# Kernel tuning notes

Measured on AMD Instinct MI355X. Metric: run time of the kernel, lower is better.

## Reference

```python
import jax, jax.numpy as jnp
import numpy as np
import math

N_ITERS = 10
N_SPIXELS = 256
NEG_INF = -1e10


def _grid_layout(h, w, n_spixels):
    # init_grid: near-square superpixel grid
    nw = int(math.sqrt(n_spixels * w / h))
    nh = int(math.sqrt(n_spixels * h / w))
    cy = np.minimum((np.arange(h) * nh) // h, nh - 1)
    cx = np.minimum((np.arange(w) * nw) // w, nw - 1)
    iy = np.broadcast_to(cy[:, None], (h, w))
    ix = np.broadcast_to(cx[None, :], (h, w))
    init_idx = iy * nw + ix  # [h,w] hard grid assignment
    # 9 candidate superpixels per pixel (3x3 neighborhood of its grid cell)
    offs = np.array([(dy, dx) for dy in (-1, 0, 1) for dx in (-1, 0, 1)])
    ny = iy[None] + offs[:, 0, None, None]  # [9,h,w]
    nx = ix[None] + offs[:, 1, None, None]
    valid = (ny >= 0) & (ny < nh) & (nx >= 0) & (nx < nw)
    nidx = np.clip(ny, 0, nh - 1) * nw + np.clip(nx, 0, nw - 1)
    return init_idx.astype(np.int32), nidx.astype(np.int32), valid, nw, nh


def setup_inputs() -> dict:
    key = jax.random.key(0)
    x = jax.random.normal(key, (2, 20, 512, 512), dtype=jnp.float32)
    return {"x": x}


def reference(x):
    b, c, h, w = x.shape
    init_idx_np, nidx_np, valid_np, nw, nh = _grid_layout(h, w, N_SPIXELS)
    K = nw * nh
    n = h * w
    init_idx = jnp.asarray(init_idx_np.reshape(n))          # [N]
    nidx = jnp.asarray(nidx_np.reshape(9, n))                # [9,N]
    valid = jnp.asarray(valid_np.reshape(9, n))              # [9,N]
    flat_nidx = nidx.reshape(-1)                             # [9N]

    pf_all = x.reshape(b, c, n)

    def init_spf(pf):  # pf [c,N] -> [c,K]: hard-assignment mean (InitSpixelFeats)
        s = jax.ops.segment_sum(pf.T, init_idx, num_segments=K)      # [K,c]
        cnt = jax.ops.segment_sum(jnp.ones((n,), pf.dtype), init_idx, num_segments=K)
        return (s / jnp.maximum(cnt, 1.0)[:, None]).T

    def calc_neg_dist(pf, spf):  # CalcAssoc: [9,N] neg sq dist to 9 neighbors
        nf = spf[:, nidx]                                    # [c,9,N]
        d = jnp.sum((pf[:, None, :] - nf) ** 2, axis=0)      # [9,N]
        return jnp.where(valid, -d, NEG_INF)

    def map_p2sp(pf, Q):  # CalcSpixelFeats: Q-weighted scatter mean, Q [9,N]
        wf = (pf[:, None, :] * Q[None]).reshape(c, -1)       # [c,9N]
        num = jax.ops.segment_sum(wf.T, flat_nidx, num_segments=K)   # [K,c]
        den = jax.ops.segment_sum(Q.reshape(-1), flat_nidx, num_segments=K)
        return (num / jnp.maximum(den, 1e-8)[:, None]).T

    def per_sample(pf):
        spf0 = init_spf(jax.lax.stop_gradient(pf))  # spf init from detached pf
        Q0 = jnp.zeros((9, n), pf.dtype)
        def body(carry, _):
            spf, _ = carry
            Q = jax.nn.softmax(calc_neg_dist(pf, spf), axis=0)
            return (map_p2sp(pf, Q), Q), None
        (spf, Q), _ = jax.lax.scan(body, (spf0, Q0), None, length=N_ITERS)
        return Q, spf

    Q, spf = jax.vmap(per_sample)(pf_all)
    return Q.reshape(b, 9, h, w), spf, x
```

## Files before the change

kernel.cpp:

```cpp
#include <hip/hip_runtime.h>

#define BATCH 2
#define C 20
#define W 512
#define NPIX (512*512)
#define NW 16
#define NH 16
#define K 256
#define NITERS 10
#define SPLIT 4
#define PITCH 260
#define NEG_INF_F (-1.0e10f)
#define REC 189
#define RECP 192

__global__ __launch_bounds__(256)
void ssn_init_kernel(const float* __restrict__ x,
                     float* __restrict__ outX,
                     float* __restrict__ buf0) {
    __shared__ float pf_tile[C][PITCH];
    __shared__ float chpart[80];
    const int t    = threadIdx.x;
    const int bi   = blockIdx.x;
    const int cell = bi & (K - 1);
    const int b    = bi >> 8;
    const int ky = cell >> 4, kx = cell & 15;
    const int py = t >> 5, px = t & 31;
    const int xcol = kx * 32 + px;

    const float* xb = x    + (size_t)b * C * NPIX;
    float*       ox = outX + (size_t)b * C * NPIX;
    float sum4[C];
#pragma unroll
    for (int ch = 0; ch < C; ++ch) sum4[ch] = 0.f;
#pragma unroll
    for (int p = 0; p < 4; ++p) {
        int y = ky * 32 + p * 8 + py;
        const float* src = xb + (size_t)y * W + xcol;
        float*       dst = ox + (size_t)y * W + xcol;
#pragma unroll
        for (int ch = 0; ch < C; ++ch) {
            float v = src[(size_t)ch * NPIX];
            sum4[ch] += v;
            dst[(size_t)ch * NPIX] = v;
        }
    }
#pragma unroll
    for (int ch = 0; ch < C; ++ch) pf_tile[ch][t] = sum4[ch];
    __syncthreads();
    if (t < 80) {
        int ch = t >> 2, q = t & 3;
        const float4* p = (const float4*)&pf_tile[ch][0];
        float s4 = 0.f;
#pragma unroll
        for (int i = 0; i < 16; ++i) {
            float4 v = p[q * 16 + i];
            s4 += v.x + v.y + v.z + v.w;
        }
        chpart[t] = s4;
    }
    __syncthreads();
    if (t < REC) {
        float v = 0.f;
        if (t >= 84 && t < 104) {
            int ch = t - 84;
            v = chpart[ch * 4] + chpart[ch * 4 + 1]
              + chpart[ch * 4 + 2] + chpart[ch * 4 + 3];
        } else if (t == 104) {
            v = 1024.0f;
        }
        float* base = buf0 + (size_t)bi * (SPLIT * RECP);
        base[t] = v;
        base[RECP + t] = 0.f;
        base[2 * RECP + t] = 0.f;
        base[3 * RECP + t] = 0.f;
    }
}

__global__ __launch_bounds__(256)
void ssn_iterate_kernel(const float* __restrict__ x,
                        const float* __restrict__ rp,
                        float* __restrict__ wp,
                        float* __restrict__ outQ,
                        int last) {
    __shared__ float spf_lds[9][C];
    __shared__ float den_lds[9];
    __shared__ float sumsq_lds[9];
    __shared__ float pf_tile[C][PITCH];
    __shared__ float w_tile[9][PITCH];

    const int t  = threadIdx.x;
    const int bi = blockIdx.x;
    const int s    = bi & 3;
    const int cell = (bi >> 2) & (K - 1);
    const int b    = bi >> 10;
    const int bcell = (b << 8) + cell;
    const int ky = cell >> 4, kx = cell & 15;
    const int py = t >> 5, px = t & 31;
    const int y  = ky * 32 + s * 8 + py;
    const int xcol = kx * 32 + px;

    float pf[C];
    const float* xb = x + (size_t)b * C * NPIX + (size_t)y * W + xcol;
#pragma unroll
    for (int ch = 0; ch < C; ++ch) pf[ch] = xb[(size_t)ch * NPIX];

    float numreg = 0.f;
    if (t < 180) {
        int jj = t / 20, ch = t % 20;
        int ny = ky + jj / 3 - 1, nx = kx + jj % 3 - 1;
        if (ny >= 0 && ny < NH && nx >= 0 && nx < NW) {
#pragma unroll
            for (int j2 = 0; j2 < 9; ++j2) {
                int cy = ny - (j2 / 3 - 1), cx = nx - (j2 % 3 - 1);
                if (cy >= 0 && cy < NH && cx >= 0 && cx < NW) {
                    const float* p = rp +
                        (size_t)((b << 8) + cy * NW + cx) * (SPLIT * RECP)
                        + j2 * 21 + ch;
#pragma unroll
                    for (int ss = 0; ss < SPLIT; ++ss)
                        numreg += p[ss * RECP];
                }
            }
        }
    }
    if (t >= 192 && t < 201) {
        int jj = t - 192;
        int ny = ky + jj / 3 - 1, nx = kx + jj % 3 - 1;
        float den = 0.f;
        if (ny >= 0 && ny < NH && nx >= 0 && nx < NW) {
#pragma unroll
            for (int j2 = 0; j2 < 9; ++j2) {
                int cy = ny - (j2 / 3 - 1), cx = nx - (j2 % 3 - 1);
                if (cy >= 0 && cy < NH && cx >= 0 && cx < NW) {
                    const float* p = rp +
                        (size_t)((b << 8) + cy * NW + cx) * (SPLIT * RECP)
                        + j2 * 21 + 20;
#pragma unroll
                    for (int ss = 0; ss < SPLIT; ++ss)
                        den += p[ss * RECP];
                }
            }
        }
        den_lds[jj] = den;
    }
    __syncthreads();
    if (t < 180) {
        int jj = t / 20, ch = t % 20;
        spf_lds[jj][ch] = numreg / fmaxf(den_lds[jj], 1e-8f);
    }
    __syncthreads();
    if (t < 9) {
        float ss2 = 0.f;
#pragma unroll
        for (int ch = 0; ch < C; ++ch) ss2 += spf_lds[t][ch] * spf_lds[t][ch];
        sumsq_lds[t] = ss2;
    }
    __syncthreads();

    float sc[9];
#pragma unroll
    for (int j = 0; j < 9; ++j) {
        int ny = ky + j / 3 - 1, nx = kx + j % 3 - 1;
        bool valid = (ny >= 0 && ny < NH && nx >= 0 && nx < NW);
        float dot = 0.f;
#pragma unroll
        for (int ch = 0; ch < C; ++ch) dot = fmaf(pf[ch], spf_lds[j][ch], dot);
        sc[j] = valid ? fmaf(2.f, dot, -sumsq_lds[j]) : NEG_INF_F;
    }
    float m = sc[0];
#pragma unroll
    for (int j = 1; j < 9; ++j) m = fmaxf(m, sc[j]);
    float wv[9], wsum = 0.f;
#pragma unroll
    for (int j = 0; j < 9; ++j) { wv[j] = __expf(sc[j] - m); wsum += wv[j]; }
    float inv = 1.0f / wsum;
#pragma unroll
    for (int j = 0; j < 9; ++j) { wv[j] *= inv; w_tile[j][t] = wv[j]; }
#pragma unroll
    for (int ch = 0; ch < C; ++ch) pf_tile[ch][t] = pf[ch];

    if (last) {
        float* q = outQ + (size_t)b * 9 * NPIX + (size_t)y * W + xcol;
#pragma unroll
        for (int j = 0; j < 9; ++j) q[(size_t)j * NPIX] = wv[j];
    }
    __syncthreads();

    if (t < 144) {
        const int tile = t >> 4, lane = t & 15;
        const int jt = tile / 3, rt = tile % 3;
        float acc[3][7];
#pragma unroll
        for (int jj = 0; jj < 3; ++jj)
#pragma unroll
            for (int rr = 0; rr < 7; ++rr) acc[jj][rr] = 0.f;

#pragma unroll
        for (int cc = 0; cc < 4; ++cc) {
            int c4 = lane + (cc << 4);
            float4 w4[3], f4[7];
#pragma unroll
            for (int jj = 0; jj < 3; ++jj)
                w4[jj] = ((const float4*)&w_tile[3 * jt + jj][0])[c4];
#pragma unroll
            for (int rr = 0; rr < 7; ++rr) {
                int r = 7 * rt + rr;
                if (r < 20) f4[rr] = ((const float4*)&pf_tile[r][0])[c4];
            }
#pragma unroll
            for (int jj = 0; jj < 3; ++jj)
#pragma unroll
                for (int rr = 0; rr < 7; ++rr) {
                    int r = 7 * rt + rr;
                    if (r < 20) {
                        acc[jj][rr] = fmaf(w4[jj].x, f4[rr].x, acc[jj][rr]);
                        acc[jj][rr] = fmaf(w4[jj].y, f4[rr].y, acc[jj][rr]);
                        acc[jj][rr] = fmaf(w4[jj].z, f4[rr].z, acc[jj][rr]);
                        acc[jj][rr] = fmaf(w4[jj].w, f4[rr].w, acc[jj][rr]);
                    } else {
                        acc[jj][rr] += w4[jj].x + w4[jj].y
                                     + w4[jj].z + w4[jj].w;
                    }
                }
        }
#pragma unroll
        for (int off = 8; off >= 1; off >>= 1)
#pragma unroll
            for (int jj = 0; jj < 3; ++jj)
#pragma unroll
                for (int rr = 0; rr < 7; ++rr)
                    acc[jj][rr] += __shfl_down(acc[jj][rr], off);
        if (lane == 0) {
            float* dst = wp + (size_t)bcell * (SPLIT * RECP) + s * RECP;
#pragma unroll
            for (int jj = 0; jj < 3; ++jj)
#pragma unroll
                for (int rr = 0; rr < 7; ++rr)
                    dst[(3 * jt + jj) * 21 + 7 * rt + rr] = acc[jj][rr];
        }
    }
}

__global__ void ssn_final_kernel(const float* __restrict__ part,
                                 float* __restrict__ outSpf) {
    int idx = blockIdx.x * blockDim.x + threadIdx.x;
    if (idx >= BATCH * K * C) return;
    int ch = idx % C;
    int k  = (idx / C) % K;
    int b  = idx / (C * K);
    int ky = k >> 4, kx = k & 15;
    float num = 0.f, den = 0.f;
#pragma unroll
    for (int j2 = 0; j2 < 9; ++j2) {
        int cy = ky - (j2 / 3 - 1), cx = kx - (j2 % 3 - 1);
        if (cy >= 0 && cy < NH && cx >= 0 && cx < NW) {
            const float* p = part +
                (size_t)((b << 8) + cy * NW + cx) * (SPLIT * RECP) + j2 * 21;
#pragma unroll
            for (int ss = 0; ss < SPLIT; ++ss) {
                num += p[ss * RECP + ch];
                den += p[ss * RECP + 20];
            }
        }
    }
    outSpf[((size_t)b * C + ch) * K + k] = num / fmaxf(den, 1e-8f);
}

extern "C" void kernel_launch(void* const* d_in, const int* in_sizes, int n_in,
                              void* d_out, int out_size, void* d_ws, size_t ws_size,
                              hipStream_t stream) {
    const float* x = (const float*)d_in[0];
    float* out = (float*)d_out;
    float* outQ   = out;
    float* outSpf = out + (size_t)BATCH * 9 * NPIX;
    float* outX   = outSpf + (size_t)BATCH * C * K;

    float* ws = (float*)d_ws;
    float* buf0 = ws;
    float* buf1 = buf0 + (size_t)BATCH * K * SPLIT * RECP;

    ssn_init_kernel<<<BATCH * K, 256, 0, stream>>>(x, outX, buf0);

    for (int it = 0; it < NITERS; ++it) {
        const float* rp = (it & 1) ? buf1 : buf0;
        float*       wp = (it & 1) ? buf0 : buf1;
        ssn_iterate_kernel<<<BATCH * K * SPLIT, 256, 0, stream>>>(
            x, rp, wp, outQ, (it == NITERS - 1) ? 1 : 0);
    }
    ssn_final_kernel<<<(BATCH * K * C + 255) / 256, 256, 0, stream>>>(
        buf0, outSpf);
}
```

Before: 299.9 us.

## Split spf reduction into separate kernel and spread x copy across iterations

Adds a small per-superpixel reduce kernel that turns the split partial sums into spf plus its sum of squares once per iteration. The iterate kernel then reads only 9 neighbour records instead of each block redundantly gathering 9x9x4 partials. The output copy of x is moved out of the init kernel and spread over the iterate kernels, each handling one tenth of the blocks while its pixels are already in registers, so the init kernel gets lighter and runs over more blocks. The cost is ten extra kernel launches and one more global round trip for spf, and the single partials buffer is now reused in place with no ping-pong.

```diff
diff --git a/kernel.cpp b/kernel.cpp
--- a/kernel.cpp
+++ b/kernel.cpp
@@ -13,88 +13,18 @@
 #define NEG_INF_F (-1.0e10f)
 #define REC 189
 #define RECP 192
+#define SPFP 32
 
 __global__ __launch_bounds__(256)
 void ssn_init_kernel(const float* __restrict__ x,
-                     float* __restrict__ outX,
-                     float* __restrict__ buf0) {
-    __shared__ float pf_tile[C][PITCH];
-    __shared__ float chpart[80];
-    const int t    = threadIdx.x;
-    const int bi   = blockIdx.x;
-    const int cell = bi & (K - 1);
-    const int b    = bi >> 8;
-    const int ky = cell >> 4, kx = cell & 15;
-    const int py = t >> 5, px = t & 31;
-    const int xcol = kx * 32 + px;
-
-    const float* xb = x    + (size_t)b * C * NPIX;
-    float*       ox = outX + (size_t)b * C * NPIX;
-    float sum4[C];
-#pragma unroll
-    for (int ch = 0; ch < C; ++ch) sum4[ch] = 0.f;
-#pragma unroll
-    for (int p = 0; p < 4; ++p) {
-        int y = ky * 32 + p * 8 + py;
-        const float* src = xb + (size_t)y * W + xcol;
-        float*       dst = ox + (size_t)y * W + xcol;
-#pragma unroll
-        for (int ch = 0; ch < C; ++ch) {
-            float v = src[(size_t)ch * NPIX];
-            sum4[ch] += v;
-            dst[(size_t)ch * NPIX] = v;
-        }
-    }
-#pragma unroll
-    for (int ch = 0; ch < C; ++ch) pf_tile[ch][t] = sum4[ch];
-    __syncthreads();
-    if (t < 80) {
-        int ch = t >> 2, q = t & 3;
-        const float4* p = (const float4*)&pf_tile[ch][0];
-        float s4 = 0.f;
-#pragma unroll
-        for (int i = 0; i < 16; ++i) {
-            float4 v = p[q * 16 + i];
-            s4 += v.x + v.y + v.z + v.w;
-        }
-        chpart[t] = s4;
-    }
-    __syncthreads();
-    if (t < REC) {
-        float v = 0.f;
-        if (t >= 84 && t < 104) {
-            int ch = t - 84;
-            v = chpart[ch * 4] + chpart[ch * 4 + 1]
-              + chpart[ch * 4 + 2] + chpart[ch * 4 + 3];
-        } else if (t == 104) {
-            v = 1024.0f;
-        }
-        float* base = buf0 + (size_t)bi * (SPLIT * RECP);
-        base[t] = v;
-        base[RECP + t] = 0.f;
-        base[2 * RECP + t] = 0.f;
-        base[3 * RECP + t] = 0.f;
-    }
-}
-
-__global__ __launch_bounds__(256)
-void ssn_iterate_kernel(const float* __restrict__ x,
-                        const float* __restrict__ rp,
-                        float* __restrict__ wp,
-                        float* __restrict__ outQ,
-                        int last) {
-    __shared__ float spf_lds[9][C];
-    __shared__ float den_lds[9];
-    __shared__ float sumsq_lds[9];
-    __shared__ float pf_tile[C][PITCH];
-    __shared__ float w_tile[9][PITCH];
-
+                     float* __restrict__ part) {
+    __shared__ float wsum[4][C];
+    __shared__ float chsum[C];
     const int t  = threadIdx.x;
     const int bi = blockIdx.x;
     const int s    = bi & 3;
     const int cell = (bi >> 2) & (K - 1);
     const int b    = bi >> 10;
-    const int bcell = (b << 8) + cell;
     const int ky = cell >> 4, kx = cell & 15;
     const int py = t >> 5, px = t & 31;
     const int y  = ky * 32 + s * 8 + py;
@@ -105,56 +35,122 @@
 #pragma unroll
     for (int ch = 0; ch < C; ++ch) pf[ch] = xb[(size_t)ch * NPIX];
 
-    float numreg = 0.f;
+    const int wid = t >> 6, lane = t & 63;
+#pragma unroll
+    for (int ch = 0; ch < C; ++ch) {
+        float v = pf[ch];
+#pragma unroll
+        for (int off = 32; off >= 1; off >>= 1) v += __shfl_down(v, off);
+        if (lane == 0) wsum[wid][ch] = v;
+    }
+    __syncthreads();
+    if (t < C) chsum[t] = wsum[0][t] + wsum[1][t] + wsum[2][t] + wsum[3][t];
+    __syncthreads();
+    if (t < REC) {
+        float v = 0.f;
+        if (t >= 84 && t < 104)      v = chsum[t - 84];
+        else if (t == 104)           v = 256.0f;
+        part[(size_t)((b << 8) + cell) * (SPLIT * RECP) + s * RECP + t] = v;
+    }
+}
+
+__global__ __launch_bounds__(64)
+void ssn_reduce_kernel(const float* __restrict__ part,
+                       float* __restrict__ spfP,
+                       float* __restrict__ outSpf,
+                       int final_mode) {
+    __shared__ float num_lds[C];
+    __shared__ float den_lds;
+    __shared__ float sq_lds[C];
+    const int t  = threadIdx.x;
+    const int bi = blockIdx.x;
+    const int cell = bi & (K - 1);
+    const int b    = bi >> 8;
+    const int ky = cell >> 4, kx = cell & 15;
+
+    if (t <= C) {
+        float acc = 0.f;
+#pragma unroll
+        for (int j2 = 0; j2 < 9; ++j2) {
+            int cy = ky - (j2 / 3 - 1), cx = kx - (j2 % 3 - 1);
+            if (cy >= 0 && cy < NH && cx >= 0 && cx < NW) {
+                const float* p = part +
+                    (size_t)((b << 8) + cy * NW + cx) * (SPLIT * RECP)
+                    + j2 * 21 + t;
+#pragma unroll
+                for (int ss = 0; ss < SPLIT; ++ss) acc += p[ss * RECP];
+            }
+        }
+        if (t < C) num_lds[t] = acc;
+        else       den_lds    = acc;
+    }
+    __syncthreads();
+    if (t < C) {
+        float v = num_lds[t] / fmaxf(den_lds, 1e-8f);
+        if (final_mode) {
+            outSpf[((size_t)b * C + t) * K + cell] = v;
+        } else {
+            spfP[(size_t)bi * SPFP + t] = v;
+            sq_lds[t] = v * v;
+        }
+    }
+    __syncthreads();
+    if (!final_mode && t == 0) {
+        float ss2 = 0.f;
+#pragma unroll
+        for (int ch = 0; ch < C; ++ch) ss2 += sq_lds[ch];
+        spfP[(size_t)bi * SPFP + C] = ss2;
+    }
+}
+
+__global__ __launch_bounds__(256)
+void ssn_iterate_kernel(const float* __restrict__ x,
+                        const float* __restrict__ spfP,
+                        float* __restrict__ wp,
+                        float* __restrict__ outX,
+                        float* __restrict__ outQ,
+                        int it, int last) {
+    __shared__ float spf_lds[9][C];
+    __shared__ float sumsq_lds[9];
+    __shared__ float pf_tile[C][PITCH];
+    __shared__ float w_tile[9][PITCH];
+
+    const int t  = threadIdx.x;
+    const int bi = blockIdx.x;
+    const int s    = bi & 3;
+    const int cell = (bi >> 2) & (K - 1);
+    const int b    = bi >> 10;
+    const int ky = cell >> 4, kx = cell & 15;
+    const int py = t >> 5, px = t & 31;
+    const int y  = ky * 32 + s * 8 + py;
+    const int xcol = kx * 32 + px;
+
+    float pf[C];
+    const size_t xoff = (size_t)b * C * NPIX + (size_t)y * W + xcol;
+    const float* xb = x + xoff;
+#pragma unroll
+    for (int ch = 0; ch < C; ++ch) pf[ch] = xb[(size_t)ch * NPIX];
+
+    if ((bi % 10) == it) {
+        float* ox = outX + xoff;
+#pragma unroll
+        for (int ch = 0; ch < C; ++ch) ox[(size_t)ch * NPIX] = pf[ch];
+    }
+
     if (t < 180) {
         int jj = t / 20, ch = t % 20;
         int ny = ky + jj / 3 - 1, nx = kx + jj % 3 - 1;
-        if (ny >= 0 && ny < NH && nx >= 0 && nx < NW) {
-#pragma unroll
-            for (int j2 = 0; j2 < 9; ++j2) {
-                int cy = ny - (j2 / 3 - 1), cx = nx - (j2 % 3 - 1);
-                if (cy >= 0 && cy < NH && cx >= 0 && cx < NW) {
-                    const float* p = rp +
-                        (size_t)((b << 8) + cy * NW + cx) * (SPLIT * RECP)
-                        + j2 * 21 + ch;
-#pragma unroll
-                    for (int ss = 0; ss < SPLIT; ++ss)
-                        numreg += p[ss * RECP];
-                }
-            }
-        }
-    }
-    if (t >= 192 && t < 201) {
-        int jj = t - 192;
+        float v = 0.f;
+        if (ny >= 0 && ny < NH && nx >= 0 && nx < NW)
+            v = spfP[(size_t)((b << 8) + ny * NW + nx) * SPFP + ch];
+        spf_lds[jj][ch] = v;
+    } else if (t < 189) {
+        int jj = t - 180;
         int ny = ky + jj / 3 - 1, nx = kx + jj % 3 - 1;
-        float den = 0.f;
-        if (ny >= 0 && ny < NH && nx >= 0 && nx < NW) {
-#pragma unroll
-            for (int j2 = 0; j2 < 9; ++j2) {
-                int cy = ny - (j2 / 3 - 1), cx = nx - (j2 % 3 - 1);
-                if (cy >= 0 && cy < NH && cx >= 0 && cx < NW) {
-                    const float* p = rp +
-                        (size_t)((b << 8) + cy * NW + cx) * (SPLIT * RECP)
-                        + j2 * 21 + 20;
-#pragma unroll
-                    for (int ss = 0; ss < SPLIT; ++ss)
-                        den += p[ss * RECP];
-                }
-            }
-        }
-        den_lds[jj] = den;
-    }
-    __syncthreads();
-    if (t < 180) {
-        int jj = t / 20, ch = t % 20;
-        spf_lds[jj][ch] = numreg / fmaxf(den_lds[jj], 1e-8f);
-    }
-    __syncthreads();
-    if (t < 9) {
-        float ss2 = 0.f;
-#pragma unroll
-        for (int ch = 0; ch < C; ++ch) ss2 += spf_lds[t][ch] * spf_lds[t][ch];
-        sumsq_lds[t] = ss2;
+        float v = 0.f;
+        if (ny >= 0 && ny < NH && nx >= 0 && nx < NW)
+            v = spfP[(size_t)((b << 8) + ny * NW + nx) * SPFP + C];
+        sumsq_lds[jj] = v;
     }
     __syncthreads();
 
@@ -232,7 +228,8 @@
                 for (int rr = 0; rr < 7; ++rr)
                     acc[jj][rr] += __shfl_down(acc[jj][rr], off);
         if (lane == 0) {
-            float* dst = wp + (size_t)bcell * (SPLIT * RECP) + s * RECP;
+            float* dst = wp + (size_t)((b << 8) + cell) * (SPLIT * RECP)
+                       + s * RECP;
 #pragma unroll
             for (int jj = 0; jj < 3; ++jj)
 #pragma unroll
@@ -240,31 +237,6 @@
                     dst[(3 * jt + jj) * 21 + 7 * rt + rr] = acc[jj][rr];
         }
     }
-}
-
-__global__ void ssn_final_kernel(const float* __restrict__ part,
-                                 float* __restrict__ outSpf) {
-    int idx = blockIdx.x * blockDim.x + threadIdx.x;
-    if (idx >= BATCH * K * C) return;
-    int ch = idx % C;
-    int k  = (idx / C) % K;
-    int b  = idx / (C * K);
-    int ky = k >> 4, kx = k & 15;
-    float num = 0.f, den = 0.f;
-#pragma unroll
-    for (int j2 = 0; j2 < 9; ++j2) {
-        int cy = ky - (j2 / 3 - 1), cx = kx - (j2 % 3 - 1);
-        if (cy >= 0 && cy < NH && cx >= 0 && cx < NW) {
-            const float* p = part +
-                (size_t)((b << 8) + cy * NW + cx) * (SPLIT * RECP) + j2 * 21;
-#pragma unroll
-            for (int ss = 0; ss < SPLIT; ++ss) {
-                num += p[ss * RECP + ch];
-                den += p[ss * RECP + 20];
-            }
-        }
-    }
-    outSpf[((size_t)b * C + ch) * K + k] = num / fmaxf(den, 1e-8f);
 }
 
 extern "C" void kernel_launch(void* const* d_in, const int* in_sizes, int n_in,
@@ -276,18 +248,19 @@
     float* outSpf = out + (size_t)BATCH * 9 * NPIX;
     float* outX   = outSpf + (size_t)BATCH * C * K;
 
-    float* ws = (float*)d_ws;
-    float* buf0 = ws;
-    float* buf1 = buf0 + (size_t)BATCH * K * SPLIT * RECP;
-
-    ssn_init_kernel<<<BATCH * K, 256, 0, stream>>>(x, outX, buf0);
+    float* ws   = (float*)d_ws;
+    float* part = ws;
+    float* spfP = part + (size_t)BATCH * K * SPLIT * RECP;
+
+    ssn_init_kernel<<<BATCH * K * SPLIT, 256, 0, stream>>>(x, part);
+    ssn_reduce_kernel<<<BATCH * K, 64, 0, stream>>>(part, spfP, nullptr, 0);
 
     for (int it = 0; it < NITERS; ++it) {
-        const float* rp = (it & 1) ? buf1 : buf0;
-        float*       wp = (it & 1) ? buf0 : buf1;
         ssn_iterate_kernel<<<BATCH * K * SPLIT, 256, 0, stream>>>(
-            x, rp, wp, outQ, (it == NITERS - 1) ? 1 : 0);
-    }
-    ssn_final_kernel<<<(BATCH * K * C + 255) / 256, 256, 0, stream>>>(
-        buf0, outSpf);
-}
+            x, spfP, part, outX, outQ, it, (it == NITERS - 1) ? 1 : 0);
+        if (it < NITERS - 1)
+            ssn_reduce_kernel<<<BATCH * K, 64, 0, stream>>>(
+                part, spfP, nullptr, 0);
+    }
+    ssn_reduce_kernel<<<BATCH * K, 64, 0, stream>>>(part, nullptr, outSpf, 1);
+}
```

Result: faster. 284.9 us (-5.0%).
